# Performance work log

Measured on AMD Instinct MI355X. Metric: run time of the kernel, lower is better.

## Reference

```python
import jax, jax.numpy as jnp
import numpy as np

N_NODES = 20000
N_EDGES = 640000
IN_CH = 128
HID = 128
NUM_GRAPHS = 64


def setup_inputs() -> dict:
    key = jax.random.key(0)
    ks = jax.random.split(key, 16)
    s_in = 1.0 / np.sqrt(IN_CH)
    s_h = 1.0 / np.sqrt(HID)
    return {
        "x": jax.random.normal(ks[0], (N_NODES, IN_CH), jnp.float32),
        "edge_index": jax.random.randint(ks[1], (2, N_EDGES), 0, N_NODES, jnp.int64),
        "batch": jnp.sort(jax.random.randint(ks[2], (N_NODES,), 0, NUM_GRAPHS, jnp.int64)),
        "W1a": jax.random.normal(ks[3], (IN_CH, HID), jnp.float32) * s_in,
        "b1a": jnp.zeros((HID,), jnp.float32),
        "W1b": jax.random.normal(ks[4], (HID, HID), jnp.float32) * s_h,
        "b1b": jnp.zeros((HID,), jnp.float32),
        "W2a": jax.random.normal(ks[5], (HID, HID), jnp.float32) * s_h,
        "b2a": jnp.zeros((HID,), jnp.float32),
        "W2b": jax.random.normal(ks[6], (HID, HID), jnp.float32) * s_h,
        "b2b": jnp.zeros((HID,), jnp.float32),
        "fc_w": jax.random.normal(ks[7], (HID, 1), jnp.float32) * s_h,
        "fc_b": jnp.zeros((1,), jnp.float32),
    }


def _gin_conv(x, edge_index, Wa, ba, Wb, bb):
    # PyG GINConv (eps=0, sum aggregation): MLP(x + scatter_add(x[src] -> dst))
    src, dst = edge_index[0], edge_index[1]
    agg = jax.ops.segment_sum(x[src], dst, num_segments=x.shape[0])
    h = x + agg
    h = jax.nn.relu(h @ Wa + ba)
    return h @ Wb + bb


def reference(x, edge_index, batch, W1a, b1a, W1b, b1b, W2a, b2a, W2b, b2b, fc_w, fc_b):
    h = jax.nn.relu(_gin_conv(x, edge_index, W1a, b1a, W1b, b1b))
    # dropout: inference mode -> identity
    h = jax.nn.relu(_gin_conv(h, edge_index, W2a, b2a, W2b, b2b))
    # global_mean_pool over graph ids
    sums = jax.ops.segment_sum(h, batch, num_segments=NUM_GRAPHS)
    counts = jax.ops.segment_sum(jnp.ones((h.shape[0],), h.dtype), batch, num_segments=NUM_GRAPHS)
    pooled = sums / jnp.maximum(counts, 1.0)[:, None]
    return pooled @ fc_w + fc_b
```

## Files before the change

### kernel.cpp

```cpp
#include <hip/hip_runtime.h>

#define NN 20000
#define NE 640000
#define CH 128
#define NG 64
#define NSLICE (NN / 8)
#define CAP 96

typedef unsigned short u16;
typedef unsigned char u8;
typedef __attribute__((ext_vector_type(8))) short short8;
typedef __attribute__((ext_vector_type(4))) float floatx4;
typedef __attribute__((ext_vector_type(2))) float floatx2;

__device__ __forceinline__ float b2f(u16 u) {
    union { float f; unsigned int i; } v; v.i = ((unsigned int)u) << 16; return v.f;
}
__device__ __forceinline__ u16 f2b(float f) {
    unsigned int u = __float_as_uint(f);
    u += 0x7fff + ((u >> 16) & 1);
    return (u16)(u >> 16);
}
__device__ __forceinline__ u8 f2q(float f) {
    return (u8)(__builtin_amdgcn_cvt_pk_fp8_f32(f, f, 0, false) & 0xff);
}

__device__ __forceinline__ void acc8(uint2 q, floatx2* a) {
    a[0] += __builtin_amdgcn_cvt_pk_f32_fp8(q.x, false);
    a[1] += __builtin_amdgcn_cvt_pk_f32_fp8(q.x, true);
    a[2] += __builtin_amdgcn_cvt_pk_f32_fp8(q.y, false);
    a[3] += __builtin_amdgcn_cvt_pk_f32_fp8(q.y, true);
}

__global__ __launch_bounds__(256) void prep(const float* __restrict__ x, u8* __restrict__ xq,
                                            const float* __restrict__ W1a, const float* __restrict__ W1b,
                                            const float* __restrict__ W2a, const float* __restrict__ W2b,
                                            u16* __restrict__ wt, float* __restrict__ gsum,
                                            const int* __restrict__ ei,
                                            int* __restrict__ cnt, int* __restrict__ ssrc) {
    int b = blockIdx.x;
    if (b < 2500) {
        int idx = (b * 256 + threadIdx.x) * 4;
        float4 v = *(const float4*)(x + idx);
        int pk = __builtin_amdgcn_cvt_pk_fp8_f32(v.x, v.y, 0, false);
        pk = __builtin_amdgcn_cvt_pk_fp8_f32(v.z, v.w, pk, true);
        *(unsigned int*)(xq + idx) = (unsigned int)pk;
    } else if (b < 2756) {
        int wi = b - 2500;
        int m = wi >> 6;
        int r = (wi & 63) * 256 + threadIdx.x;
        int j = r & 7, l16 = (r >> 3) & 15, quad = (r >> 7) & 3;
        int kc = (r >> 9) & 3, ct = (r >> 11) & 7;
        int n = ct * 16 + l16, k = kc * 32 + quad * 8 + j;
        const float* W = (m == 0) ? W1a : (m == 1) ? W1b : (m == 2) ? W2a : W2b;
        wt[m * 16384 + r] = f2b(W[k * 128 + n]);
    } else if (b < 2788) {
        gsum[(b - 2756) * 256 + threadIdx.x] = 0.f;
    } else {
        int idx = b - 2788;
        int slice = idx & 7, chunk = idx >> 3;
        int lo = slice * NSLICE, hi = lo + NSLICE;
        int e0 = chunk * 1250, e1 = e0 + 1250;
        for (int e = e0 + threadIdx.x; e < e1; e += 256) {
            int dst = ei[NE + e];
            if (dst >= lo && dst < hi) {
                int pos = atomicAdd(&cnt[dst], 1);
                if (pos < CAP) ssrc[dst * CAP + pos] = ei[e];
            }
        }
    }
}

__global__ __launch_bounds__(256) void agg_fp8(const u8* __restrict__ in, u16* __restrict__ out,
                                               const int* __restrict__ cnt, const int* __restrict__ ssrc) {
    int n = (blockIdx.x * 256 + threadIdx.x) >> 6;
    int lane = threadIdx.x & 63;
    int slot = lane >> 4, cg = lane & 15;
    int boff = cg * 8;
    floatx2 acc[4];
    #pragma unroll
    for (int j = 0; j < 4; ++j) acc[j] = (floatx2)(0.f);
    if (slot == 0) {
        uint2 q = *(const uint2*)(in + (size_t)n * CH + boff);
        acc8(q, acc);
    }
    int deg = cnt[n]; if (deg > CAP) deg = CAP;
    int b = n * CAP, e = b + deg;
    int base = b;
    for (; base + 16 <= e; base += 16) {
        int4 si = *(const int4*)&ssrc[base + slot * 4];
        uint2 q0 = *(const uint2*)(in + (size_t)si.x * CH + boff);
        uint2 q1 = *(const uint2*)(in + (size_t)si.y * CH + boff);
        uint2 q2 = *(const uint2*)(in + (size_t)si.z * CH + boff);
        uint2 q3 = *(const uint2*)(in + (size_t)si.w * CH + boff);
        acc8(q0, acc); acc8(q1, acc); acc8(q2, acc); acc8(q3, acc);
    }
    if (base < e) {
        int i0 = base + slot * 4;
        int4 si = *(const int4*)&ssrc[i0];
        bool ok0 = i0 + 0 < e, ok1 = i0 + 1 < e, ok2 = i0 + 2 < e, ok3 = i0 + 3 < e;
        int s0 = ok0 ? si.x : 0, s1 = ok1 ? si.y : 0, s2 = ok2 ? si.z : 0, s3 = ok3 ? si.w : 0;
        uint2 q0 = *(const uint2*)(in + (size_t)s0 * CH + boff);
        uint2 q1 = *(const uint2*)(in + (size_t)s1 * CH + boff);
        uint2 q2 = *(const uint2*)(in + (size_t)s2 * CH + boff);
        uint2 q3 = *(const uint2*)(in + (size_t)s3 * CH + boff);
        if (!ok0) q0 = make_uint2(0, 0);
        if (!ok1) q1 = make_uint2(0, 0);
        if (!ok2) q2 = make_uint2(0, 0);
        if (!ok3) q3 = make_uint2(0, 0);
        acc8(q0, acc); acc8(q1, acc); acc8(q2, acc); acc8(q3, acc);
    }
    float f[8];
    #pragma unroll
    for (int j = 0; j < 4; ++j) { f[2 * j] = acc[j][0]; f[2 * j + 1] = acc[j][1]; }
    #pragma unroll
    for (int j = 0; j < 8; ++j) {
        f[j] += __shfl_xor(f[j], 16);
        f[j] += __shfl_xor(f[j], 32);
    }
    if (slot == 0) {
        short8 o;
        #pragma unroll
        for (int j = 0; j < 8; ++j) o[j] = (short)f2b(f[j]);
        *(short8*)(out + (size_t)n * CH + boff) = o;
    }
}

template <int DO_POOL>
__global__ __launch_bounds__(256) void mlp_fused(const u16* __restrict__ A,
                                                 const u16* __restrict__ wtA, const u16* __restrict__ wtB,
                                                 const float* __restrict__ biasA, const float* __restrict__ biasB,
                                                 u8* __restrict__ outq,
                                                 const int* __restrict__ batch, float* __restrict__ gsum) {
    __shared__ u16 H[64 * 136];
    __shared__ float gacc[DO_POOL ? NG * CH : 1];
    __shared__ int sgl[2];
    int t = threadIdx.x, wave = t >> 6, lane = t & 63;
    int quad = lane >> 4, l16 = lane & 15;
    int rowblk = blockIdx.x * 64;
    int row0 = rowblk + wave * 16;

    int gg[4];
    if (DO_POOL) {
        if (t == 0) {
            sgl[0] = batch[min(rowblk, NN - 1)];
            sgl[1] = batch[min(rowblk + 63, NN - 1)];
        }
        #pragma unroll
        for (int r = 0; r < 4; ++r)
            gg[r] = batch[min(row0 + quad * 4 + r, NN - 1)];
        __syncthreads();
        int glo = sgl[0], span = (sgl[1] - glo + 1) * CH;
        for (int i = t; i < span; i += 256) gacc[glo * CH + i] = 0.f;
        __syncthreads();
    }

    short8 af[4];
    {
        int r = row0 + l16; if (r >= NN) r = NN - 1;
        #pragma unroll
        for (int kc = 0; kc < 4; ++kc)
            af[kc] = *(const short8*)(A + (size_t)r * CH + kc * 32 + quad * 8);
    }

    #pragma unroll
    for (int ct = 0; ct < 8; ++ct) {
        floatx4 a0 = (floatx4)(0.f);
        #pragma unroll
        for (int kc = 0; kc < 4; ++kc) {
            short8 bf = *(const short8*)(wtA + (((ct * 4 + kc) * 4 + quad) * 16 + l16) * 8);
            a0 = __builtin_amdgcn_mfma_f32_16x16x32_bf16(af[kc], bf, a0, 0, 0, 0);
        }
        float bv = biasA[ct * 16 + l16];
        #pragma unroll
        for (int r = 0; r < 4; ++r) {
            int lr = wave * 16 + quad * 4 + r;
            H[lr * 136 + ct * 16 + l16] = f2b(fmaxf(a0[r] + bv, 0.f));
        }
    }

    short8 af2[4];
    #pragma unroll
    for (int kc = 0; kc < 4; ++kc)
        af2[kc] = *(const short8*)&H[(wave * 16 + l16) * 136 + kc * 32 + quad * 8];

    #pragma unroll
    for (int ct = 0; ct < 8; ++ct) {
        floatx4 a0 = (floatx4)(0.f);
        #pragma unroll
        for (int kc = 0; kc < 4; ++kc) {
            short8 bf = *(const short8*)(wtB + (((ct * 4 + kc) * 4 + quad) * 16 + l16) * 8);
            a0 = __builtin_amdgcn_mfma_f32_16x16x32_bf16(af2[kc], bf, a0, 0, 0, 0);
        }
        int col = ct * 16 + l16;
        float bv = biasB[col];
        #pragma unroll
        for (int r = 0; r < 4; ++r) {
            int row = row0 + quad * 4 + r;
            if (row < NN) {
                float v = fmaxf(a0[r] + bv, 0.f);
                if (DO_POOL) atomicAdd(&gacc[gg[r] * CH + col], v);
                else outq[(size_t)row * CH + col] = f2q(v);
            }
        }
    }

    if (DO_POOL) {
        __syncthreads();
        int glo = sgl[0], ghi = sgl[1];
        int span = (ghi - glo + 1) * CH;
        for (int i = t; i < span; i += 256)
            atomicAdd(&gsum[glo * CH + i], gacc[glo * CH + i]);
    }
}

__global__ __launch_bounds__(128) void pool_final(const float* __restrict__ gsum, const int* __restrict__ batch,
                                                  const float* __restrict__ fcw, const float* __restrict__ fcb,
                                                  float* __restrict__ outp) {
    int g = blockIdx.x, t = threadIdx.x;
    __shared__ int se[2];
    if (t < 2) {
        int target = g + t, lo = 0, hi = NN;
        while (lo < hi) { int mid = (lo + hi) >> 1; if (batch[mid] < target) lo = mid + 1; else hi = mid; }
        se[t] = lo;
    }
    __syncthreads();
    int cnt = se[1] - se[0]; if (cnt < 1) cnt = 1;
    float v = gsum[g * CH + t] * fcw[t] / (float)cnt;
    __shared__ float red[128];
    red[t] = v; __syncthreads();
    for (int s = 64; s > 0; s >>= 1) { if (t < s) red[t] += red[t + s]; __syncthreads(); }
    if (t == 0) outp[g] = red[0] + fcb[0];
}

extern "C" void kernel_launch(void* const* d_in, const int* in_sizes, int n_in,
                              void* d_out, int out_size, void* d_ws, size_t ws_size,
                              hipStream_t stream) {
    const float* x   = (const float*)d_in[0];
    const int*   ei  = (const int*)d_in[1];
    const int* batch = (const int*)d_in[2];
    const float* W1a = (const float*)d_in[3];
    const float* b1a = (const float*)d_in[4];
    const float* W1b = (const float*)d_in[5];
    const float* b1b = (const float*)d_in[6];
    const float* W2a = (const float*)d_in[7];
    const float* b2a = (const float*)d_in[8];
    const float* W2b = (const float*)d_in[9];
    const float* b2b = (const float*)d_in[10];
    const float* fcw = (const float*)d_in[11];
    const float* fcb = (const float*)d_in[12];
    float* out = (float*)d_out;

    char* w = (char*)d_ws;
    u8*  xq   = (u8*)w;  w += (size_t)NN * CH;
    u8*  hq   = (u8*)w;  w += (size_t)NN * CH;
    u16* bufA = (u16*)w; w += (size_t)NN * CH * 2;
    u16* wt   = (u16*)w; w += (size_t)4 * 16384 * 2;
    int* cnt  = (int*)w; w += (size_t)NN * 4;
    float* gsum = (float*)w; w += (size_t)NG * CH * 4;
    int* ssrc = (int*)w; w += (size_t)NN * CAP * 4;

    hipMemsetAsync(cnt, 0, (size_t)NN * 4, stream);

    prep<<<6884, 256, 0, stream>>>(x, xq, W1a, W1b, W2a, W2b, wt, gsum, ei, cnt, ssrc);

    agg_fp8<<<5000, 256, 0, stream>>>(xq, bufA, cnt, ssrc);
    mlp_fused<0><<<313, 256, 0, stream>>>(bufA, wt + 0 * 16384, wt + 1 * 16384, b1a, b1b, hq, batch, gsum);
    agg_fp8<<<5000, 256, 0, stream>>>(hq, bufA, cnt, ssrc);
    mlp_fused<1><<<313, 256, 0, stream>>>(bufA, wt + 2 * 16384, wt + 3 * 16384, b2a, b2b, hq, batch, gsum);
    pool_final<<<NG, 128, 0, stream>>>(gsum, batch, fcw, fcb, out);
}
```

Measured before the change: 190.4 us.

## Fuse neighbor aggregation into per-layer MLP kernel with 16-node blocks

Merges the FP8 gather-aggregate kernel and the two-GEMM MLP kernel into a single per-layer kernel. Each block first aggregates 16 nodes into shared memory as bf16, then runs both MFMA GEMMs with the four waves splitting the output column tiles. This drops the bf16 intermediate buffer round trip through global memory and two kernel launches. In exchange, each block now reloads the full weight matrices for only 16 rows, which adds L2 traffic. Pooling blocks also reserve the large shared accumulator per block, which may limit occupancy.

```diff
diff --git a/kernel.cpp b/kernel.cpp
--- a/kernel.cpp
+++ b/kernel.cpp
@@ -13,9 +13,6 @@
 typedef __attribute__((ext_vector_type(4))) float floatx4;
 typedef __attribute__((ext_vector_type(2))) float floatx2;
 
-__device__ __forceinline__ float b2f(u16 u) {
-    union { float f; unsigned int i; } v; v.i = ((unsigned int)u) << 16; return v.f;
-}
 __device__ __forceinline__ u16 f2b(float f) {
     unsigned int u = __float_as_uint(f);
     u += 0x7fff + ((u >> 16) & 1);
@@ -24,7 +21,6 @@
 __device__ __forceinline__ u8 f2q(float f) {
     return (u8)(__builtin_amdgcn_cvt_pk_fp8_f32(f, f, 0, false) & 0xff);
 }
-
 __device__ __forceinline__ void acc8(uint2 q, floatx2* a) {
     a[0] += __builtin_amdgcn_cvt_pk_f32_fp8(q.x, false);
     a[1] += __builtin_amdgcn_cvt_pk_f32_fp8(q.x, true);
@@ -71,100 +67,95 @@
     }
 }
 
-__global__ __launch_bounds__(256) void agg_fp8(const u8* __restrict__ in, u16* __restrict__ out,
-                                               const int* __restrict__ cnt, const int* __restrict__ ssrc) {
-    int n = (blockIdx.x * 256 + threadIdx.x) >> 6;
-    int lane = threadIdx.x & 63;
-    int slot = lane >> 4, cg = lane & 15;
-    int boff = cg * 8;
-    floatx2 acc[4];
-    #pragma unroll
-    for (int j = 0; j < 4; ++j) acc[j] = (floatx2)(0.f);
-    if (slot == 0) {
-        uint2 q = *(const uint2*)(in + (size_t)n * CH + boff);
-        acc8(q, acc);
-    }
-    int deg = cnt[n]; if (deg > CAP) deg = CAP;
-    int b = n * CAP, e = b + deg;
-    int base = b;
-    for (; base + 16 <= e; base += 16) {
-        int4 si = *(const int4*)&ssrc[base + slot * 4];
-        uint2 q0 = *(const uint2*)(in + (size_t)si.x * CH + boff);
-        uint2 q1 = *(const uint2*)(in + (size_t)si.y * CH + boff);
-        uint2 q2 = *(const uint2*)(in + (size_t)si.z * CH + boff);
-        uint2 q3 = *(const uint2*)(in + (size_t)si.w * CH + boff);
-        acc8(q0, acc); acc8(q1, acc); acc8(q2, acc); acc8(q3, acc);
-    }
-    if (base < e) {
-        int i0 = base + slot * 4;
-        int4 si = *(const int4*)&ssrc[i0];
-        bool ok0 = i0 + 0 < e, ok1 = i0 + 1 < e, ok2 = i0 + 2 < e, ok3 = i0 + 3 < e;
-        int s0 = ok0 ? si.x : 0, s1 = ok1 ? si.y : 0, s2 = ok2 ? si.z : 0, s3 = ok3 ? si.w : 0;
-        uint2 q0 = *(const uint2*)(in + (size_t)s0 * CH + boff);
-        uint2 q1 = *(const uint2*)(in + (size_t)s1 * CH + boff);
-        uint2 q2 = *(const uint2*)(in + (size_t)s2 * CH + boff);
-        uint2 q3 = *(const uint2*)(in + (size_t)s3 * CH + boff);
-        if (!ok0) q0 = make_uint2(0, 0);
-        if (!ok1) q1 = make_uint2(0, 0);
-        if (!ok2) q2 = make_uint2(0, 0);
-        if (!ok3) q3 = make_uint2(0, 0);
-        acc8(q0, acc); acc8(q1, acc); acc8(q2, acc); acc8(q3, acc);
-    }
-    float f[8];
-    #pragma unroll
-    for (int j = 0; j < 4; ++j) { f[2 * j] = acc[j][0]; f[2 * j + 1] = acc[j][1]; }
-    #pragma unroll
-    for (int j = 0; j < 8; ++j) {
-        f[j] += __shfl_xor(f[j], 16);
-        f[j] += __shfl_xor(f[j], 32);
-    }
-    if (slot == 0) {
-        short8 o;
-        #pragma unroll
-        for (int j = 0; j < 8; ++j) o[j] = (short)f2b(f[j]);
-        *(short8*)(out + (size_t)n * CH + boff) = o;
-    }
-}
-
 template <int DO_POOL>
-__global__ __launch_bounds__(256) void mlp_fused(const u16* __restrict__ A,
-                                                 const u16* __restrict__ wtA, const u16* __restrict__ wtB,
-                                                 const float* __restrict__ biasA, const float* __restrict__ biasB,
-                                                 u8* __restrict__ outq,
-                                                 const int* __restrict__ batch, float* __restrict__ gsum) {
-    __shared__ u16 H[64 * 136];
+__global__ __launch_bounds__(256) void layer(const u8* __restrict__ in,
+                                             const int* __restrict__ cnt, const int* __restrict__ ssrc,
+                                             const u16* __restrict__ wtA, const u16* __restrict__ wtB,
+                                             const float* __restrict__ biasA, const float* __restrict__ biasB,
+                                             u8* __restrict__ outq,
+                                             const int* __restrict__ batch, float* __restrict__ gsum) {
+    __shared__ u16 A[16 * 136];
+    __shared__ u16 H[16 * 136];
     __shared__ float gacc[DO_POOL ? NG * CH : 1];
     __shared__ int sgl[2];
     int t = threadIdx.x, wave = t >> 6, lane = t & 63;
     int quad = lane >> 4, l16 = lane & 15;
-    int rowblk = blockIdx.x * 64;
-    int row0 = rowblk + wave * 16;
+    int nb = blockIdx.x * 16;
 
     int gg[4];
     if (DO_POOL) {
-        if (t == 0) {
-            sgl[0] = batch[min(rowblk, NN - 1)];
-            sgl[1] = batch[min(rowblk + 63, NN - 1)];
-        }
+        if (t == 0) { sgl[0] = batch[nb]; sgl[1] = batch[nb + 15]; }
         #pragma unroll
         for (int r = 0; r < 4; ++r)
-            gg[r] = batch[min(row0 + quad * 4 + r, NN - 1)];
+            gg[r] = batch[nb + quad * 4 + r];
         __syncthreads();
         int glo = sgl[0], span = (sgl[1] - glo + 1) * CH;
         for (int i = t; i < span; i += 256) gacc[glo * CH + i] = 0.f;
-        __syncthreads();
-    }
+    }
+
+    int slot = lane >> 4, cg = lane & 15;
+    int boff = cg * 8;
+    #pragma unroll
+    for (int k = 0; k < 4; ++k) {
+        int n = nb + wave * 4 + k;
+        floatx2 acc[4];
+        #pragma unroll
+        for (int j = 0; j < 4; ++j) acc[j] = (floatx2)(0.f);
+        if (slot == 0) {
+            uint2 q = *(const uint2*)(in + (size_t)n * CH + boff);
+            acc8(q, acc);
+        }
+        int deg = cnt[n]; if (deg > CAP) deg = CAP;
+        int b0 = n * CAP, e = b0 + deg;
+        int base = b0;
+        for (; base + 16 <= e; base += 16) {
+            int4 si = *(const int4*)&ssrc[base + slot * 4];
+            uint2 q0 = *(const uint2*)(in + (size_t)si.x * CH + boff);
+            uint2 q1 = *(const uint2*)(in + (size_t)si.y * CH + boff);
+            uint2 q2 = *(const uint2*)(in + (size_t)si.z * CH + boff);
+            uint2 q3 = *(const uint2*)(in + (size_t)si.w * CH + boff);
+            acc8(q0, acc); acc8(q1, acc); acc8(q2, acc); acc8(q3, acc);
+        }
+        if (base < e) {
+            int i0 = base + slot * 4;
+            int4 si = *(const int4*)&ssrc[i0];
+            bool ok0 = i0 + 0 < e, ok1 = i0 + 1 < e, ok2 = i0 + 2 < e, ok3 = i0 + 3 < e;
+            int s0 = ok0 ? si.x : 0, s1 = ok1 ? si.y : 0, s2 = ok2 ? si.z : 0, s3 = ok3 ? si.w : 0;
+            uint2 q0 = *(const uint2*)(in + (size_t)s0 * CH + boff);
+            uint2 q1 = *(const uint2*)(in + (size_t)s1 * CH + boff);
+            uint2 q2 = *(const uint2*)(in + (size_t)s2 * CH + boff);
+            uint2 q3 = *(const uint2*)(in + (size_t)s3 * CH + boff);
+            if (!ok0) q0 = make_uint2(0, 0);
+            if (!ok1) q1 = make_uint2(0, 0);
+            if (!ok2) q2 = make_uint2(0, 0);
+            if (!ok3) q3 = make_uint2(0, 0);
+            acc8(q0, acc); acc8(q1, acc); acc8(q2, acc); acc8(q3, acc);
+        }
+        float f[8];
+        #pragma unroll
+        for (int j = 0; j < 4; ++j) { f[2 * j] = acc[j][0]; f[2 * j + 1] = acc[j][1]; }
+        #pragma unroll
+        for (int j = 0; j < 8; ++j) {
+            f[j] += __shfl_xor(f[j], 16);
+            f[j] += __shfl_xor(f[j], 32);
+        }
+        if (slot == 0) {
+            short8 o;
+            #pragma unroll
+            for (int j = 0; j < 8; ++j) o[j] = (short)f2b(f[j]);
+            *(short8*)&A[(wave * 4 + k) * 136 + boff] = o;
+        }
+    }
+    __syncthreads();
 
     short8 af[4];
-    {
-        int r = row0 + l16; if (r >= NN) r = NN - 1;
-        #pragma unroll
-        for (int kc = 0; kc < 4; ++kc)
-            af[kc] = *(const short8*)(A + (size_t)r * CH + kc * 32 + quad * 8);
-    }
-
-    #pragma unroll
-    for (int ct = 0; ct < 8; ++ct) {
+    #pragma unroll
+    for (int kc = 0; kc < 4; ++kc)
+        af[kc] = *(const short8*)&A[l16 * 136 + kc * 32 + quad * 8];
+
+    #pragma unroll
+    for (int half = 0; half < 2; ++half) {
+        int ct = wave + half * 4;
         floatx4 a0 = (floatx4)(0.f);
         #pragma unroll
         for (int kc = 0; kc < 4; ++kc) {
@@ -173,19 +164,19 @@
         }
         float bv = biasA[ct * 16 + l16];
         #pragma unroll
-        for (int r = 0; r < 4; ++r) {
-            int lr = wave * 16 + quad * 4 + r;
-            H[lr * 136 + ct * 16 + l16] = f2b(fmaxf(a0[r] + bv, 0.f));
-        }
-    }
+        for (int r = 0; r < 4; ++r)
+            H[(quad * 4 + r) * 136 + ct * 16 + l16] = f2b(fmaxf(a0[r] + bv, 0.f));
+    }
+    __syncthreads();
 
     short8 af2[4];
     #pragma unroll
     for (int kc = 0; kc < 4; ++kc)
-        af2[kc] = *(const short8*)&H[(wave * 16 + l16) * 136 + kc * 32 + quad * 8];
-
-    #pragma unroll
-    for (int ct = 0; ct < 8; ++ct) {
+        af2[kc] = *(const short8*)&H[l16 * 136 + kc * 32 + quad * 8];
+
+    #pragma unroll
+    for (int half = 0; half < 2; ++half) {
+        int ct = wave + half * 4;
         floatx4 a0 = (floatx4)(0.f);
         #pragma unroll
         for (int kc = 0; kc < 4; ++kc) {
@@ -196,12 +187,10 @@
         float bv = biasB[col];
         #pragma unroll
         for (int r = 0; r < 4; ++r) {
-            int row = row0 + quad * 4 + r;
-            if (row < NN) {
-                float v = fmaxf(a0[r] + bv, 0.f);
-                if (DO_POOL) atomicAdd(&gacc[gg[r] * CH + col], v);
-                else outq[(size_t)row * CH + col] = f2q(v);
-            }
+            int row = nb + quad * 4 + r;
+            float v = fmaxf(a0[r] + bv, 0.f);
+            if (DO_POOL) atomicAdd(&gacc[gg[r] * CH + col], v);
+            else outq[(size_t)row * CH + col] = f2q(v);
         }
     }
 
@@ -254,7 +243,6 @@
     char* w = (char*)d_ws;
     u8*  xq   = (u8*)w;  w += (size_t)NN * CH;
     u8*  hq   = (u8*)w;  w += (size_t)NN * CH;
-    u16* bufA = (u16*)w; w += (size_t)NN * CH * 2;
     u16* wt   = (u16*)w; w += (size_t)4 * 16384 * 2;
     int* cnt  = (int*)w; w += (size_t)NN * 4;
     float* gsum = (float*)w; w += (size_t)NG * CH * 4;
@@ -264,9 +252,8 @@
 
     prep<<<6884, 256, 0, stream>>>(x, xq, W1a, W1b, W2a, W2b, wt, gsum, ei, cnt, ssrc);
 
-    agg_fp8<<<5000, 256, 0, stream>>>(xq, bufA, cnt, ssrc);
-    mlp_fused<0><<<313, 256, 0, stream>>>(bufA, wt + 0 * 16384, wt + 1 * 16384, b1a, b1b, hq, batch, gsum);
-    agg_fp8<<<5000, 256, 0, stream>>>(hq, bufA, cnt, ssrc);
-    mlp_fused<1><<<313, 256, 0, stream>>>(bufA, wt + 2 * 16384, wt + 3 * 16384, b2a, b2b, hq, batch, gsum);
+    layer<0><<<1250, 256, 0, stream>>>(xq, cnt, ssrc, wt + 0 * 16384, wt + 1 * 16384, b1a, b1b, hq, batch, gsum);
+    layer<1><<<1250, 256, 0, stream>>>(hq, cnt, ssrc, wt + 2 * 16384, wt + 3 * 16384, b2a, b2b, hq, batch, gsum);
+
     pool_final<<<NG, 128, 0, stream>>>(gsum, batch, fcw, fcb, out);
 }
```

After: 185.7 us. 2.5% less time.
